# Performance work log

Hardware: AMD Instinct MI355X
Metric: run time of the kernel (lower is better)

Reference implementation:

```python
import jax, jax.numpy as jnp
import numpy as np

N_NODES = 500_000
HIDDEN = 256
NUM_CLASSES = 104
AUX_DIM = 2
NUM_GRAPHS = 2048
GRAPH_X = 128
BN_EPS = 1e-5


def setup_inputs() -> dict:
    key = jax.random.key(0)
    ks = jax.random.split(key, 16)
    D_in = NUM_CLASSES + AUX_DIM  # batchnorm / feed_forward input dim
    return {
        "initial_node_states": jax.random.normal(ks[0], (N_NODES, HIDDEN), jnp.float32),
        "final_node_states": jax.random.normal(ks[1], (N_NODES, HIDDEN), jnp.float32),
        "aux_variables": jax.random.normal(ks[2], (NUM_GRAPHS, AUX_DIM), jnp.float32),
        "graph_nodes_list": jnp.sort(jax.random.randint(ks[3], (N_NODES,), 0, NUM_GRAPHS)),
        "num_graphs": NUM_GRAPHS,
        "Wg": jax.random.normal(ks[4], (2 * HIDDEN, NUM_CLASSES), jnp.float32) * 0.02,
        "bg": jnp.zeros((NUM_CLASSES,), jnp.float32),
        "Wt": jax.random.normal(ks[5], (HIDDEN, NUM_CLASSES), jnp.float32) * 0.02,
        "bt": jnp.zeros((NUM_CLASSES,), jnp.float32),
        # BatchNorm1d(initial_size) in eval mode
        "bn_gamma": jnp.ones((D_in,), jnp.float32),
        "bn_beta": jnp.zeros((D_in,), jnp.float32),
        "bn_mean": jnp.zeros((D_in,), jnp.float32),
        "bn_var": jnp.ones((D_in,), jnp.float32),
        # feed_forward: Linear(D_in -> GRAPH_X) -> ReLU -> Linear(GRAPH_X -> C)
        "W1": jax.random.normal(ks[6], (D_in, GRAPH_X), jnp.float32) * 0.05,
        "b1": jnp.zeros((GRAPH_X,), jnp.float32),
        "W2": jax.random.normal(ks[7], (GRAPH_X, NUM_CLASSES), jnp.float32) * 0.05,
        "b2": jnp.zeros((NUM_CLASSES,), jnp.float32),
    }


def reference(initial_node_states, final_node_states, aux_variables, graph_nodes_list,
              num_graphs, Wg, bg, Wt, bt, bn_gamma, bn_beta, bn_mean, bn_var,
              W1, b1, W2, b2):
    # Gated nodewise readout (pooling_method == 'default').
    gate_input = jnp.concatenate([initial_node_states, final_node_states], axis=-1)  # [N, 2H]
    gate = jax.nn.sigmoid(gate_input @ Wg + bg)                                      # [N, C]
    nodewise = gate * (final_node_states @ Wt + bt)                                  # [N, C]
    # index_add scatter pooling to per-graph buckets.
    graph_readout = jax.ops.segment_sum(nodewise, graph_nodes_list,
                                        num_segments=num_graphs)                     # [G, C]
    ext = jnp.concatenate([graph_readout, aux_variables], axis=1)                    # [G, C+A]
    # BatchNorm1d (eval mode: running statistics).
    norm = (ext - bn_mean) * jax.lax.rsqrt(bn_var + BN_EPS) * bn_gamma + bn_beta
    # feed_forward MLP (dropout disabled).
    h = jax.nn.relu(norm @ W1 + b1)
    logits = h @ W2 + b2                                                             # [G, C]
    return logits
```

## Files before the change

### kernel.cpp

```cpp
#include <hip/hip_runtime.h>
#include <hip/hip_bf16.h>

#define N_NODES   500000
#define HIDDEN    256
#define NCLASS    104
#define NGRAPH    2048
#define NCHUNK    15625
#define CPAD      112

typedef __attribute__((ext_vector_type(8))) __bf16 bf16x8;
typedef __attribute__((ext_vector_type(8))) unsigned short ushort8;
typedef __attribute__((ext_vector_type(4))) float floatx4;

__device__ __forceinline__ unsigned short f2bf(float f) {
    unsigned u = __float_as_uint(f);
    u += 0x7fffu + ((u >> 16) & 1u);
    return (unsigned short)(u >> 16);
}

__global__ void prep_kernel(const float* __restrict__ Wg, const float* __restrict__ Wt,
                            unsigned short* __restrict__ WgT, unsigned short* __restrict__ WtT) {
    int id = blockIdx.x * 256 + threadIdx.x;
    if (id < CPAD * 512) {
        int c = id >> 9, k = id & 511;
        float v = (c < NCLASS) ? Wg[k * NCLASS + c] : 0.f;
        WgT[id] = f2bf(v);
    } else {
        int id2 = id - CPAD * 512;
        int c = id2 >> 8, k = id2 & 255;
        float v = (c < NCLASS) ? Wt[k * NCLASS + c] : 0.f;
        WtT[id2] = f2bf(v);
    }
}

__device__ __forceinline__ void load_chunk(const float* __restrict__ init_s,
                                           const float* __restrict__ fin_s,
                                           int chunk, int w, int lane, float4 (&pre)[4][2]) {
    const int nb = chunk * 32;
#pragma unroll
    for (int p = 0; p < 4; ++p) {
        const int node = nb + p * 8 + w;
        const float* src = (lane < 32)
            ? (init_s + (size_t)node * HIDDEN + lane * 8)
            : (fin_s  + (size_t)node * HIDDEN + (lane - 32) * 8);
        pre[p][0] = *(const float4*)(src);
        pre[p][1] = *(const float4*)(src + 4);
    }
}

__global__ __launch_bounds__(512, 2)
void node_kernel(const float* __restrict__ init_s, const float* __restrict__ fin_s,
                 const int* __restrict__ gl, const float* __restrict__ bg,
                 const float* __restrict__ bt,
                 const unsigned short* __restrict__ WgT,
                 const unsigned short* __restrict__ WtT,
                 float* __restrict__ readout)
{
    __shared__ unsigned short Atile[2][32 * 512];

    const int tid  = threadIdx.x;
    const int lane = tid & 63;
    const int w    = tid >> 6;
    const int l15  = lane & 15;
    const int quad = lane >> 4;
    const int col  = w * 16 + l15;

    bf16x8 Bg[16], Bt[8];
    float bgv = 0.f, btv = 0.f;
    if (w < 7) {
        const int cc = (col < NCLASS) ? col : (NCLASS - 1);
        bgv = bg[cc]; btv = bt[cc];
        const unsigned short* wg = WgT + col * 512 + quad * 8;
#pragma unroll
        for (int s = 0; s < 16; ++s) Bg[s] = *(const bf16x8*)(wg + s * 32);
        const unsigned short* wt = WtT + col * 256 + quad * 8;
#pragma unroll
        for (int s = 0; s < 8; ++s)  Bt[s] = *(const bf16x8*)(wt + s * 32);
    }

    const int G = gridDim.x;
    int c = blockIdx.x;
    float4 pre[4][2];
    if (c < NCHUNK) load_chunk(init_s, fin_s, c, w, lane, pre);

    int buf = 0;
    for (; c < NCHUNK; c += G) {
#pragma unroll
        for (int p = 0; p < 4; ++p) {
            const int r  = p * 8 + w;
            const int kp = (lane * 8) ^ ((r & 7) * 8);
            ushort8 t;
            t[0] = f2bf(pre[p][0].x); t[1] = f2bf(pre[p][0].y);
            t[2] = f2bf(pre[p][0].z); t[3] = f2bf(pre[p][0].w);
            t[4] = f2bf(pre[p][1].x); t[5] = f2bf(pre[p][1].y);
            t[6] = f2bf(pre[p][1].z); t[7] = f2bf(pre[p][1].w);
            *reinterpret_cast<ushort8*>(&Atile[buf][r * 512 + kp]) = t;
        }
        const int nxt = c + G;
        if (nxt < NCHUNK) load_chunk(init_s, fin_s, nxt, w, lane, pre);

        __syncthreads();

        if (w < 7) {
            floatx4 accg0 = {0.f,0.f,0.f,0.f}, accg1 = {0.f,0.f,0.f,0.f};
            floatx4 acct0 = {0.f,0.f,0.f,0.f}, acct1 = {0.f,0.f,0.f,0.f};
            const unsigned short* Ab = &Atile[buf][0];
#pragma unroll
            for (int s = 0; s < 16; ++s) {
                const int kk = s * 32 + quad * 8;
                const int r0 = l15,      kp0 = kk ^ ((r0 & 7) * 8);
                const int r1 = 16 + l15, kp1 = kk ^ ((r1 & 7) * 8);
                bf16x8 a0 = *reinterpret_cast<const bf16x8*>(Ab + r0 * 512 + kp0);
                bf16x8 a1 = *reinterpret_cast<const bf16x8*>(Ab + r1 * 512 + kp1);
                accg0 = __builtin_amdgcn_mfma_f32_16x16x32_bf16(a0, Bg[s], accg0, 0, 0, 0);
                accg1 = __builtin_amdgcn_mfma_f32_16x16x32_bf16(a1, Bg[s], accg1, 0, 0, 0);
                if (s >= 8) {
                    acct0 = __builtin_amdgcn_mfma_f32_16x16x32_bf16(a0, Bt[s - 8], acct0, 0, 0, 0);
                    acct1 = __builtin_amdgcn_mfma_f32_16x16x32_bf16(a1, Bt[s - 8], acct1, 0, 0, 0);
                }
            }
#pragma unroll
            for (int rc = 0; rc < 2; ++rc) {
                const floatx4 ag = rc ? accg1 : accg0;
                const floatx4 at = rc ? acct1 : acct0;
                const int nb = c * 32 + rc * 16;
                float vals[4];
#pragma unroll
                for (int j = 0; j < 4; ++j) {
                    const float sg = 1.f / (1.f + __expf(-(ag[j] + bgv)));
                    vals[j] = sg * (at[j] + btv);
                }
                const int gfirst = gl[nb];
                const int glast  = gl[nb + 15];
                if (gfirst == glast) {
                    float v = vals[0] + vals[1] + vals[2] + vals[3];
                    v += __shfl_xor(v, 16, 64);
                    v += __shfl_xor(v, 32, 64);
                    if (quad == 0 && col < NCLASS)
                        atomicAdd(&readout[gfirst * NCLASS + col], v);
                } else {
#pragma unroll
                    for (int j = 0; j < 4; ++j) {
                        const int node = nb + quad * 4 + j;
                        const int g = gl[node];
                        if (col < NCLASS)
                            atomicAdd(&readout[g * NCLASS + col], vals[j]);
                    }
                }
            }
        }
        buf ^= 1;
    }
}

__global__ __launch_bounds__(128)
void mlp_kernel(const float* __restrict__ readout, const float* __restrict__ aux,
                const float* __restrict__ gamma, const float* __restrict__ beta,
                const float* __restrict__ mean, const float* __restrict__ var,
                const float* __restrict__ W1, const float* __restrict__ b1,
                const float* __restrict__ W2, const float* __restrict__ b2,
                float* __restrict__ out)
{
    __shared__ float xs[8][112];
    __shared__ float hs[8][128];
    const int g0 = blockIdx.x * 8;
    const int tid = threadIdx.x;

    for (int v = tid; v < 8 * 106; v += 128) {
        const int r = v / 106, i = v - r * 106;
        const float raw = (i < NCLASS) ? readout[(g0 + r) * NCLASS + i]
                                       : aux[(g0 + r) * 2 + (i - NCLASS)];
        xs[r][i] = (raw - mean[i]) * rsqrtf(var[i] + 1e-5f) * gamma[i] + beta[i];
    }
    __syncthreads();
    {
        const int j = tid;
        float acc[8];
#pragma unroll
        for (int r = 0; r < 8; ++r) acc[r] = b1[j];
        for (int i = 0; i < 106; ++i) {
            const float ww = W1[i * 128 + j];
#pragma unroll
            for (int r = 0; r < 8; ++r) acc[r] += xs[r][i] * ww;
        }
#pragma unroll
        for (int r = 0; r < 8; ++r) hs[r][j] = fmaxf(acc[r], 0.f);
    }
    __syncthreads();
    if (tid < NCLASS) {
        float acc[8];
#pragma unroll
        for (int r = 0; r < 8; ++r) acc[r] = b2[tid];
        for (int j = 0; j < 128; ++j) {
            const float ww = W2[j * NCLASS + tid];
#pragma unroll
            for (int r = 0; r < 8; ++r) acc[r] += hs[r][j] * ww;
        }
#pragma unroll
        for (int r = 0; r < 8; ++r) out[(g0 + r) * NCLASS + tid] = acc[r];
    }
}

extern "C" void kernel_launch(void* const* d_in, const int* in_sizes, int n_in,
                              void* d_out, int out_size, void* d_ws, size_t ws_size,
                              hipStream_t stream) {
    const float* init_s = (const float*)d_in[0];
    const float* fin_s  = (const float*)d_in[1];
    const float* aux    = (const float*)d_in[2];
    const int*   gl     = (const int*)d_in[3];
    const float* Wg = (const float*)d_in[5];
    const float* bg = (const float*)d_in[6];
    const float* Wt = (const float*)d_in[7];
    const float* bt = (const float*)d_in[8];
    const float* bn_gamma = (const float*)d_in[9];
    const float* bn_beta  = (const float*)d_in[10];
    const float* bn_mean  = (const float*)d_in[11];
    const float* bn_var   = (const float*)d_in[12];
    const float* W1 = (const float*)d_in[13];
    const float* b1 = (const float*)d_in[14];
    const float* W2 = (const float*)d_in[15];
    const float* b2 = (const float*)d_in[16];
    float* out = (float*)d_out;

    char* ws = (char*)d_ws;
    float* readout      = (float*)ws;
    unsigned short* WgT = (unsigned short*)(ws + 851968);
    unsigned short* WtT = (unsigned short*)(ws + 851968 + 114688);

    hipMemsetAsync(readout, 0, NGRAPH * NCLASS * sizeof(float), stream);
    prep_kernel<<<336, 256, 0, stream>>>(Wg, Wt, WgT, WtT);
    node_kernel<<<256, 512, 0, stream>>>(init_s, fin_s, gl, bg, bt, WgT, WtT, readout);
    mlp_kernel<<<NGRAPH / 8, 128, 0, stream>>>(readout, aux, bn_gamma, bn_beta,
                                               bn_mean, bn_var, W1, b1, W2, b2, out);
}
```

Baseline: 1.033 ms.

## Keep weights in LDS and give each wave its own 16-node tile with register A fragments

The node kernel is restructured. The weight matrices now sit in padded LDS, and each wave loads its own 16-row activation tile straight into registers as MFMA A fragments, looping over all 7 column tiles. This drops the shared A-tile staging, the per-chunk __syncthreads and the idle eighth wave, so every wave streams input independently. In exchange the weight fragments are re-read from LDS for every tile, register pressure rises (16 bf16x8 fragments plus 32 float4 loads), and the one-chunk-ahead prefetch of the next inputs is gone.

```diff
diff --git a/kernel.cpp b/kernel.cpp
--- a/kernel.cpp
+++ b/kernel.cpp
@@ -5,8 +5,9 @@
 #define HIDDEN    256
 #define NCLASS    104
 #define NGRAPH    2048
-#define NCHUNK    15625
-#define CPAD      112
+#define NTILE     31250
+#define WG_STRIDE 520
+#define WT_STRIDE 264
 
 typedef __attribute__((ext_vector_type(8))) __bf16 bf16x8;
 typedef __attribute__((ext_vector_type(8))) unsigned short ushort8;
@@ -21,30 +22,13 @@
 __global__ void prep_kernel(const float* __restrict__ Wg, const float* __restrict__ Wt,
                             unsigned short* __restrict__ WgT, unsigned short* __restrict__ WtT) {
     int id = blockIdx.x * 256 + threadIdx.x;
-    if (id < CPAD * 512) {
+    if (id < NCLASS * 512) {
         int c = id >> 9, k = id & 511;
-        float v = (c < NCLASS) ? Wg[k * NCLASS + c] : 0.f;
-        WgT[id] = f2bf(v);
+        WgT[id] = f2bf(Wg[k * NCLASS + c]);
     } else {
-        int id2 = id - CPAD * 512;
+        int id2 = id - NCLASS * 512;
         int c = id2 >> 8, k = id2 & 255;
-        float v = (c < NCLASS) ? Wt[k * NCLASS + c] : 0.f;
-        WtT[id2] = f2bf(v);
-    }
-}
-
-__device__ __forceinline__ void load_chunk(const float* __restrict__ init_s,
-                                           const float* __restrict__ fin_s,
-                                           int chunk, int w, int lane, float4 (&pre)[4][2]) {
-    const int nb = chunk * 32;
-#pragma unroll
-    for (int p = 0; p < 4; ++p) {
-        const int node = nb + p * 8 + w;
-        const float* src = (lane < 32)
-            ? (init_s + (size_t)node * HIDDEN + lane * 8)
-            : (fin_s  + (size_t)node * HIDDEN + (lane - 32) * 8);
-        pre[p][0] = *(const float4*)(src);
-        pre[p][1] = *(const float4*)(src + 4);
+        WtT[id2] = f2bf(Wt[k * NCLASS + c]);
     }
 }
 
@@ -56,100 +40,103 @@
                  const unsigned short* __restrict__ WtT,
                  float* __restrict__ readout)
 {
-    __shared__ unsigned short Atile[2][32 * 512];
+    __shared__ unsigned short Bg_lds[NCLASS * WG_STRIDE];
+    __shared__ unsigned short Bt_lds[NCLASS * WT_STRIDE];
 
     const int tid  = threadIdx.x;
     const int lane = tid & 63;
     const int w    = tid >> 6;
     const int l15  = lane & 15;
     const int quad = lane >> 4;
-    const int col  = w * 16 + l15;
-
-    bf16x8 Bg[16], Bt[8];
-    float bgv = 0.f, btv = 0.f;
-    if (w < 7) {
-        const int cc = (col < NCLASS) ? col : (NCLASS - 1);
-        bgv = bg[cc]; btv = bt[cc];
-        const unsigned short* wg = WgT + col * 512 + quad * 8;
-#pragma unroll
-        for (int s = 0; s < 16; ++s) Bg[s] = *(const bf16x8*)(wg + s * 32);
-        const unsigned short* wt = WtT + col * 256 + quad * 8;
-#pragma unroll
-        for (int s = 0; s < 8; ++s)  Bt[s] = *(const bf16x8*)(wt + s * 32);
-    }
-
-    const int G = gridDim.x;
-    int c = blockIdx.x;
-    float4 pre[4][2];
-    if (c < NCHUNK) load_chunk(init_s, fin_s, c, w, lane, pre);
-
-    int buf = 0;
-    for (; c < NCHUNK; c += G) {
-#pragma unroll
-        for (int p = 0; p < 4; ++p) {
-            const int r  = p * 8 + w;
-            const int kp = (lane * 8) ^ ((r & 7) * 8);
-            ushort8 t;
-            t[0] = f2bf(pre[p][0].x); t[1] = f2bf(pre[p][0].y);
-            t[2] = f2bf(pre[p][0].z); t[3] = f2bf(pre[p][0].w);
-            t[4] = f2bf(pre[p][1].x); t[5] = f2bf(pre[p][1].y);
-            t[6] = f2bf(pre[p][1].z); t[7] = f2bf(pre[p][1].w);
-            *reinterpret_cast<ushort8*>(&Atile[buf][r * 512 + kp]) = t;
-        }
-        const int nxt = c + G;
-        if (nxt < NCHUNK) load_chunk(init_s, fin_s, nxt, w, lane, pre);
-
-        __syncthreads();
-
-        if (w < 7) {
-            floatx4 accg0 = {0.f,0.f,0.f,0.f}, accg1 = {0.f,0.f,0.f,0.f};
-            floatx4 acct0 = {0.f,0.f,0.f,0.f}, acct1 = {0.f,0.f,0.f,0.f};
-            const unsigned short* Ab = &Atile[buf][0];
+
+    for (int i = tid; i < NCLASS * 512 / 8; i += 512) {
+        const int c = (i * 8) >> 9, k = (i * 8) & 511;
+        *reinterpret_cast<ushort8*>(&Bg_lds[c * WG_STRIDE + k]) =
+            *reinterpret_cast<const ushort8*>(&WgT[c * 512 + k]);
+    }
+    for (int i = tid; i < NCLASS * 256 / 8; i += 512) {
+        const int c = (i * 8) >> 8, k = (i * 8) & 255;
+        *reinterpret_cast<ushort8*>(&Bt_lds[c * WT_STRIDE + k]) =
+            *reinterpret_cast<const ushort8*>(&WtT[c * 256 + k]);
+    }
+
+    float bgv[7], btv[7];
+#pragma unroll
+    for (int ct = 0; ct < 7; ++ct) {
+        int c = ct * 16 + l15; if (c > NCLASS - 1) c = NCLASS - 1;
+        bgv[ct] = bg[c]; btv[ct] = bt[c];
+    }
+
+    __syncthreads();
+
+    const int wid = blockIdx.x * 8 + w;
+
+    for (int t = wid; t < NTILE; t += 2048) {
+        const int row = t * 16 + l15;
+        const float* pi = init_s + (size_t)row * HIDDEN + quad * 8;
+        const float* pf = fin_s  + (size_t)row * HIDDEN + quad * 8;
+        float4 v[16][2];
+#pragma unroll
+        for (int s = 0; s < 8; ++s) {
+            v[s][0]     = *reinterpret_cast<const float4*>(pi + s * 32);
+            v[s][1]     = *reinterpret_cast<const float4*>(pi + s * 32 + 4);
+            v[s + 8][0] = *reinterpret_cast<const float4*>(pf + s * 32);
+            v[s + 8][1] = *reinterpret_cast<const float4*>(pf + s * 32 + 4);
+        }
+        bf16x8 a[16];
+#pragma unroll
+        for (int s = 0; s < 16; ++s) {
+            ushort8 u;
+            u[0] = f2bf(v[s][0].x); u[1] = f2bf(v[s][0].y);
+            u[2] = f2bf(v[s][0].z); u[3] = f2bf(v[s][0].w);
+            u[4] = f2bf(v[s][1].x); u[5] = f2bf(v[s][1].y);
+            u[6] = f2bf(v[s][1].z); u[7] = f2bf(v[s][1].w);
+            a[s] = __builtin_bit_cast(bf16x8, u);
+        }
+
+        const int gfirst = gl[t * 16];
+        const int glast  = gl[t * 16 + 15];
+
+#pragma unroll
+        for (int ct = 0; ct < 7; ++ct) {
+            int cb = ct * 16 + l15; if (cb > NCLASS - 1) cb = NCLASS - 1;
+            const unsigned short* bgp = &Bg_lds[cb * WG_STRIDE + quad * 8];
+            const unsigned short* btp = &Bt_lds[cb * WT_STRIDE + quad * 8];
+            floatx4 accg = {0.f, 0.f, 0.f, 0.f};
+            floatx4 acct = {0.f, 0.f, 0.f, 0.f};
 #pragma unroll
             for (int s = 0; s < 16; ++s) {
-                const int kk = s * 32 + quad * 8;
-                const int r0 = l15,      kp0 = kk ^ ((r0 & 7) * 8);
-                const int r1 = 16 + l15, kp1 = kk ^ ((r1 & 7) * 8);
-                bf16x8 a0 = *reinterpret_cast<const bf16x8*>(Ab + r0 * 512 + kp0);
-                bf16x8 a1 = *reinterpret_cast<const bf16x8*>(Ab + r1 * 512 + kp1);
-                accg0 = __builtin_amdgcn_mfma_f32_16x16x32_bf16(a0, Bg[s], accg0, 0, 0, 0);
-                accg1 = __builtin_amdgcn_mfma_f32_16x16x32_bf16(a1, Bg[s], accg1, 0, 0, 0);
-                if (s >= 8) {
-                    acct0 = __builtin_amdgcn_mfma_f32_16x16x32_bf16(a0, Bt[s - 8], acct0, 0, 0, 0);
-                    acct1 = __builtin_amdgcn_mfma_f32_16x16x32_bf16(a1, Bt[s - 8], acct1, 0, 0, 0);
-                }
-            }
-#pragma unroll
-            for (int rc = 0; rc < 2; ++rc) {
-                const floatx4 ag = rc ? accg1 : accg0;
-                const floatx4 at = rc ? acct1 : acct0;
-                const int nb = c * 32 + rc * 16;
-                float vals[4];
-#pragma unroll
-                for (int j = 0; j < 4; ++j) {
-                    const float sg = 1.f / (1.f + __expf(-(ag[j] + bgv)));
-                    vals[j] = sg * (at[j] + btv);
-                }
-                const int gfirst = gl[nb];
-                const int glast  = gl[nb + 15];
-                if (gfirst == glast) {
-                    float v = vals[0] + vals[1] + vals[2] + vals[3];
-                    v += __shfl_xor(v, 16, 64);
-                    v += __shfl_xor(v, 32, 64);
-                    if (quad == 0 && col < NCLASS)
-                        atomicAdd(&readout[gfirst * NCLASS + col], v);
-                } else {
+                bf16x8 bfrag = *reinterpret_cast<const bf16x8*>(bgp + s * 32);
+                accg = __builtin_amdgcn_mfma_f32_16x16x32_bf16(a[s], bfrag, accg, 0, 0, 0);
+            }
+#pragma unroll
+            for (int s = 0; s < 8; ++s) {
+                bf16x8 bfrag = *reinterpret_cast<const bf16x8*>(btp + s * 32);
+                acct = __builtin_amdgcn_mfma_f32_16x16x32_bf16(a[s + 8], bfrag, acct, 0, 0, 0);
+            }
+            float vals[4];
+#pragma unroll
+            for (int j = 0; j < 4; ++j) {
+                const float sg = 1.f / (1.f + __expf(-(accg[j] + bgv[ct])));
+                vals[j] = sg * (acct[j] + btv[ct]);
+            }
+            const int col = ct * 16 + l15;
+            if (gfirst == glast) {
+                float vsum = vals[0] + vals[1] + vals[2] + vals[3];
+                vsum += __shfl_xor(vsum, 16, 64);
+                vsum += __shfl_xor(vsum, 32, 64);
+                if (quad == 0 && col < NCLASS)
+                    atomicAdd(&readout[gfirst * NCLASS + col], vsum);
+            } else {
+                if (col < NCLASS) {
 #pragma unroll
                     for (int j = 0; j < 4; ++j) {
-                        const int node = nb + quad * 4 + j;
-                        const int g = gl[node];
-                        if (col < NCLASS)
-                            atomicAdd(&readout[g * NCLASS + col], vals[j]);
+                        const int g = gl[t * 16 + quad * 4 + j];
+                        atomicAdd(&readout[g * NCLASS + col], vals[j]);
                     }
                 }
             }
         }
-        buf ^= 1;
     }
 }
 
@@ -225,10 +212,10 @@
     char* ws = (char*)d_ws;
     float* readout      = (float*)ws;
     unsigned short* WgT = (unsigned short*)(ws + 851968);
-    unsigned short* WtT = (unsigned short*)(ws + 851968 + 114688);
+    unsigned short* WtT = (unsigned short*)(ws + 851968 + 106496);
 
     hipMemsetAsync(readout, 0, NGRAPH * NCLASS * sizeof(float), stream);
-    prep_kernel<<<336, 256, 0, stream>>>(Wg, Wt, WgT, WtT);
+    prep_kernel<<<312, 256, 0, stream>>>(Wg, Wt, WgT, WtT);
     node_kernel<<<256, 512, 0, stream>>>(init_s, fin_s, gl, bg, bt, WgT, WtT, readout);
     mlp_kernel<<<NGRAPH / 8, 128, 0, stream>>>(readout, aux, bn_gamma, bn_beta,
                                                bn_mean, bn_var, W1, b1, W2, b2, out);
```

After: 2.301 ms. 2.23x slower.
